# Performance work log

Measured on AMD Instinct MI355X. Metric: run time of the kernel, lower is better.

Reference implementation:

```python
import jax, jax.numpy as jnp
import numpy as np

BS1, BS2, NUM_EC = 32, 128, 64
CONV_DIM, MEM_DIM, MLP_DIM = 64, 256, 256
Q_DIM = 4 * CONV_DIM  # query_dim of criteria


def setup_inputs() -> dict:
    key = jax.random.key(0)
    k = jax.random.split(key, 6)
    in_dim = Q_DIM + MEM_DIM
    s_a = 1.0 / np.sqrt(in_dim)
    return {
        "ehr_vector": jax.random.normal(k[0], (BS2, MEM_DIM), dtype=jnp.float32),
        "criteria": jax.random.normal(k[1], (BS1, NUM_EC, Q_DIM), dtype=jnp.float32),
        "ec_mask": jnp.ones((BS1, NUM_EC), dtype=jnp.float32),
        # alignment: Linear(mem_dim + 4*conv_dim, 1) -> store as [in_dim] vector + scalar bias
        "W_align": jax.random.normal(k[2], (in_dim,), dtype=jnp.float32) * s_a,
        "b_align": jax.random.normal(k[3], (1,), dtype=jnp.float32) * s_a,
        # mlp: Linear(mem_dim + 4*conv_dim, mlp_dim) -> store as [in_dim, mlp_dim]
        "W_mlp": jax.random.normal(k[4], (in_dim, MLP_DIM), dtype=jnp.float32) * s_a,
        "b_mlp": jax.random.normal(k[5], (MLP_DIM,), dtype=jnp.float32) * s_a,
    }


def reference(ehr_vector, criteria, ec_mask, W_align, b_align, W_mlp, b_mlp):
    # Math identical to: att = softmax(Linear(cat[criteria, ehr]), dim=ec);
    # h = Linear_mlp(cat[criteria, ehr] * att). Concat is never materialized:
    # split both linear weights along the input dim instead.
    q = criteria.shape[-1]
    Wa_c, Wa_e = W_align[:q], W_align[q:]
    # additive attention logits: [bs1, bs2, num_ec]
    logit_c = jnp.einsum("beq,q->be", criteria, Wa_c)      # [bs1, num_ec]
    logit_e = jnp.einsum("pm,m->p", ehr_vector, Wa_e)      # [bs2]
    logits = logit_c[:, None, :] + logit_e[None, :, None] + b_align[0]
    att = jax.nn.softmax(logits, axis=2)                   # softmax over num_ec

    Wm_c, Wm_e = W_mlp[:q], W_mlp[q:]
    proj_c = jnp.einsum("beq,qd->bed", criteria, Wm_c)     # [bs1, num_ec, mlp]
    proj_e = jnp.einsum("pm,md->pd", ehr_vector, Wm_e)     # [bs2, mlp]
    # mlp((cat * att)) = att * (cat @ W_mlp) + b_mlp  (att is scalar per (b,p,e))
    h = att[..., None] * (proj_c[:, None, :, :] + proj_e[None, :, None, :]) + b_mlp
    return h  # [bs1, bs2, num_ec, mlp_dim]
```

## Files before the change

### kernel.cpp

```cpp
#include <hip/hip_runtime.h>

#define BS1 32
#define BS2 128
#define NEC 64
#define QD  256
#define MD  256

__global__ __launch_bounds__(256)
void prep_kernel(const float* __restrict__ crit,
                 const float* __restrict__ ehr,
                 const float* __restrict__ w_mlp,
                 const float* __restrict__ w_align,
                 float* __restrict__ proj_c,
                 float* __restrict__ proj_e,
                 float* __restrict__ att) {
    __shared__ float smem[8 * QD];
    __shared__ float logits[NEC];
    int tid = threadIdx.x;
    int blk = blockIdx.x;

    if (blk < 272) {
        const float* A; const float* B; float* out; int m0;
        if (blk < 256) { A = crit; B = w_mlp;           out = proj_c; m0 = blk * 8; }
        else           { A = ehr;  B = w_mlp + QD * MD; out = proj_e; m0 = (blk - 256) * 8; }
        {
            const float* src = A + m0 * QD + tid * 8;
            float4 a0 = *(const float4*)src;
            float4 a1 = *(const float4*)(src + 4);
            *(float4*)&smem[tid * 8]     = a0;
            *(float4*)&smem[tid * 8 + 4] = a1;
        }
        __syncthreads();
        int r = tid >> 5;
        int c = (tid & 31) * 8;
        float acc[8] = {0.f,0.f,0.f,0.f,0.f,0.f,0.f,0.f};
        #pragma unroll 4
        for (int k = 0; k < QD; ++k) {
            float a = smem[r * QD + k];
            const float* bp = B + k * MD + c;
            float4 b0 = *(const float4*)bp;
            float4 b1 = *(const float4*)(bp + 4);
            acc[0] = fmaf(a, b0.x, acc[0]);
            acc[1] = fmaf(a, b0.y, acc[1]);
            acc[2] = fmaf(a, b0.z, acc[2]);
            acc[3] = fmaf(a, b0.w, acc[3]);
            acc[4] = fmaf(a, b1.x, acc[4]);
            acc[5] = fmaf(a, b1.y, acc[5]);
            acc[6] = fmaf(a, b1.z, acc[6]);
            acc[7] = fmaf(a, b1.w, acc[7]);
        }
        float* o = out + (m0 + r) * MD + c;
        *(float4*)o       = make_float4(acc[0], acc[1], acc[2], acc[3]);
        *(float4*)(o + 4) = make_float4(acc[4], acc[5], acc[6], acc[7]);
    } else {
        int b = blk - 272;
        smem[tid] = w_align[tid];
        __syncthreads();
        int e = tid >> 2, q = tid & 3;
        const float* row = crit + (b * NEC + e) * QD + q * 64;
        const float* w   = &smem[q * 64];
        float acc = 0.f;
        #pragma unroll
        for (int k = 0; k < 64; k += 4) {
            float4 u = *(const float4*)(row + k);
            acc = fmaf(u.x, w[k + 0], acc);
            acc = fmaf(u.y, w[k + 1], acc);
            acc = fmaf(u.z, w[k + 2], acc);
            acc = fmaf(u.w, w[k + 3], acc);
        }
        acc += __shfl_xor(acc, 1);
        acc += __shfl_xor(acc, 2);
        if (q == 0) logits[e] = acc;
        __syncthreads();
        if (tid < NEC) {
            float l = logits[tid];
            float m = l;
            #pragma unroll
            for (int off = 32; off; off >>= 1) m = fmaxf(m, __shfl_xor(m, off));
            float ex = __expf(l - m);
            float s = ex;
            #pragma unroll
            for (int off = 32; off; off >>= 1) s += __shfl_xor(s, off);
            att[b * NEC + tid] = ex / s;
        }
    }
}

__global__ __launch_bounds__(256)
void final_kernel(const float* __restrict__ att,
                  const float* __restrict__ proj_c,
                  const float* __restrict__ proj_e,
                  const float* __restrict__ b_mlp,
                  float*       __restrict__ out) {
    int tid = threadIdx.x;
    int bp  = blockIdx.x;
    int b = bp >> 7, p = bp & 127;
    int wid = tid >> 6;
    int d   = (tid & 63) * 4;

    const float4 pe = *(const float4*)(proj_e + p * MD + d);
    const float4 bm = *(const float4*)(b_mlp + d);

    const float* attp = att + b * NEC + wid;
    float a[16];
    #pragma unroll
    for (int pass = 0; pass < 16; ++pass) a[pass] = attp[pass * 4];

    const float* pc = proj_c + (b * NEC + wid) * MD + d;
    float*       o  = out + (size_t)bp * (NEC * MD) + tid * 4;

    #pragma unroll
    for (int pass = 0; pass < 16; ++pass) {
        float4 c0 = *(const float4*)pc;
        float4 r0;
        r0.x = fmaf(a[pass], c0.x + pe.x, bm.x);
        r0.y = fmaf(a[pass], c0.y + pe.y, bm.y);
        r0.z = fmaf(a[pass], c0.z + pe.z, bm.z);
        r0.w = fmaf(a[pass], c0.w + pe.w, bm.w);
        *(float4*)o = r0;
        pc += 4 * MD;
        o  += 1024;
    }
}

extern "C" void kernel_launch(void* const* d_in, const int* in_sizes, int n_in,
                              void* d_out, int out_size, void* d_ws, size_t ws_size,
                              hipStream_t stream) {
    const float* ehr     = (const float*)d_in[0];
    const float* crit    = (const float*)d_in[1];
    const float* w_align = (const float*)d_in[3];
    const float* w_mlp   = (const float*)d_in[5];
    const float* b_mlp   = (const float*)d_in[6];
    float* out = (float*)d_out;

    float* att    = (float*)d_ws;
    float* proj_c = att + BS1 * NEC;
    float* proj_e = proj_c + BS1 * NEC * MD;

    prep_kernel<<<272 + BS1, 256, 0, stream>>>(crit, ehr, w_mlp, w_align,
                                               proj_c, proj_e, att);
    final_kernel<<<BS1 * BS2, 256, 0, stream>>>(att, proj_c, proj_e, b_mlp, out);
}
```

Baseline: 308.8 us.

## Fuse prep and output kernels into one cooperative launch with grid sync

Replaces the two-kernel sequence with a single cooperative kernel of 1024 blocks. The blocks first compute the projections, with the GEMM split into 4-row tiles to spread it over more blocks, plus the attention softmax. After a grid-wide sync, each block writes four (b,p) output slabs. This removes the second launch and the gap between kernels. In exchange it adds a grid barrier and fixes the output phase at 1024 resident blocks, and it falls back to the old two-kernel path if the cooperative launch fails.

```diff
diff --git a/kernel.cpp b/kernel.cpp
--- a/kernel.cpp
+++ b/kernel.cpp
@@ -1,10 +1,117 @@
 #include <hip/hip_runtime.h>
+#include <hip/hip_cooperative_groups.h>
+
+namespace cg = cooperative_groups;
 
 #define BS1 32
 #define BS2 128
 #define NEC 64
 #define QD  256
 #define MD  256
+
+__global__ __launch_bounds__(256, 4)
+void fused_kernel(const float* __restrict__ crit,
+                  const float* __restrict__ ehr,
+                  const float* __restrict__ w_mlp,
+                  const float* __restrict__ w_align,
+                  const float* __restrict__ b_mlp,
+                  float* __restrict__ proj_c,
+                  float* __restrict__ proj_e,
+                  float* __restrict__ att,
+                  float* __restrict__ out) {
+    __shared__ float As[4 * QD];
+    __shared__ float logits[NEC];
+    int tid = threadIdx.x;
+    int blk = blockIdx.x;
+
+    if (blk < 544) {
+        const float* A; const float* B; float* outp; int m0;
+        if (blk < 512) { A = crit; B = w_mlp;           outp = proj_c; m0 = blk * 4; }
+        else           { A = ehr;  B = w_mlp + QD * MD; outp = proj_e; m0 = (blk - 512) * 4; }
+        *(float4*)&As[tid * 4] = *(const float4*)(A + m0 * QD + tid * 4);
+        __syncthreads();
+        int r = tid >> 6;
+        int c = (tid & 63) * 4;
+        float acc[4] = {0.f, 0.f, 0.f, 0.f};
+        #pragma unroll 4
+        for (int k = 0; k < QD; ++k) {
+            float a = As[r * QD + k];
+            float4 b0 = *(const float4*)(B + k * MD + c);
+            acc[0] = fmaf(a, b0.x, acc[0]);
+            acc[1] = fmaf(a, b0.y, acc[1]);
+            acc[2] = fmaf(a, b0.z, acc[2]);
+            acc[3] = fmaf(a, b0.w, acc[3]);
+        }
+        *(float4*)(outp + (m0 + r) * MD + c) =
+            make_float4(acc[0], acc[1], acc[2], acc[3]);
+    } else if (blk < 576) {
+        int b = blk - 544;
+        As[tid] = w_align[tid];
+        __syncthreads();
+        int e = tid >> 2, q = tid & 3;
+        const float* row = crit + (b * NEC + e) * QD + q * 64;
+        const float* w   = &As[q * 64];
+        float acc = 0.f;
+        #pragma unroll
+        for (int k = 0; k < 64; k += 4) {
+            float4 u = *(const float4*)(row + k);
+            acc = fmaf(u.x, w[k + 0], acc);
+            acc = fmaf(u.y, w[k + 1], acc);
+            acc = fmaf(u.z, w[k + 2], acc);
+            acc = fmaf(u.w, w[k + 3], acc);
+        }
+        acc += __shfl_xor(acc, 1);
+        acc += __shfl_xor(acc, 2);
+        if (q == 0) logits[e] = acc;
+        __syncthreads();
+        if (tid < NEC) {
+            float l = logits[tid];
+            float m = l;
+            #pragma unroll
+            for (int off = 32; off; off >>= 1) m = fmaxf(m, __shfl_xor(m, off));
+            float ex = __expf(l - m);
+            float s = ex;
+            #pragma unroll
+            for (int off = 32; off; off >>= 1) s += __shfl_xor(s, off);
+            att[b * NEC + tid] = ex / s;
+        }
+    }
+
+    __threadfence();
+    cg::this_grid().sync();
+
+    int wid = tid >> 6;
+    int d   = (tid & 63) * 4;
+    #pragma unroll
+    for (int i = 0; i < 4; ++i) {
+        int bp = blk + i * 1024;
+        int b = bp >> 7, p = bp & 127;
+
+        const float4 pe = *(const float4*)(proj_e + p * MD + d);
+        const float4 bm = *(const float4*)(b_mlp + d);
+
+        const float* attp = att + b * NEC + wid;
+        float a[16];
+        #pragma unroll
+        for (int pass = 0; pass < 16; ++pass) a[pass] = attp[pass * 4];
+
+        const float* pc = proj_c + (b * NEC + wid) * MD + d;
+        float*       o  = out + (size_t)bp * (NEC * MD) + tid * 4;
+
+        #pragma unroll
+        for (int pass = 0; pass < 16; ++pass) {
+            float4 c0 = *(const float4*)pc;
+            float4 r0;
+            r0.x = fmaf(a[pass], c0.x + pe.x, bm.x);
+            r0.y = fmaf(a[pass], c0.y + pe.y, bm.y);
+            r0.z = fmaf(a[pass], c0.z + pe.z, bm.z);
+            r0.w = fmaf(a[pass], c0.w + pe.w, bm.w);
+            *(float4*)o = r0;
+            pc += 4 * MD;
+            o  += 1024;
+        }
+    }
+}
 
 __global__ __launch_bounds__(256)
 void prep_kernel(const float* __restrict__ crit,
@@ -137,7 +244,16 @@
     float* proj_c = att + BS1 * NEC;
     float* proj_e = proj_c + BS1 * NEC * MD;
 
-    prep_kernel<<<272 + BS1, 256, 0, stream>>>(crit, ehr, w_mlp, w_align,
-                                               proj_c, proj_e, att);
-    final_kernel<<<BS1 * BS2, 256, 0, stream>>>(att, proj_c, proj_e, b_mlp, out);
-}
+    void* args[] = { (void*)&crit, (void*)&ehr, (void*)&w_mlp, (void*)&w_align,
+                     (void*)&b_mlp, (void*)&proj_c, (void*)&proj_e, (void*)&att,
+                     (void*)&out };
+    hipError_t err = hipLaunchCooperativeKernel((void*)fused_kernel,
+                                                dim3(1024), dim3(256),
+                                                args, 0, stream);
+    if (err != hipSuccess) {
+        (void)hipGetLastError();
+        prep_kernel<<<272 + BS1, 256, 0, stream>>>(crit, ehr, w_mlp, w_align,
+                                                   proj_c, proj_e, att);
+        final_kernel<<<BS1 * BS2, 256, 0, stream>>>(att, proj_c, proj_e, b_mlp, out);
+    }
+}
```

New measurement: 511.9 us. +65.8%, slower.

## Remap final kernel blocks to (batch, criterion) and iterate over patients

Applied to the files above, without the earlier changes.

The final kernel's grid changes from one block per (b,p) to one block per (b,e), giving 2048 blocks instead of 4096. Each block computes att*proj_c+b_mlp once and loops over the 128 proj_e rows, four patients per group. This cuts the per-element work to one FMA and reuses the attention scalar and proj_c row from registers. The trade-off is that each wave's output stores now land in rows strided by NEC*MD rather than in one contiguous block, which may hurt write coalescing in this store-bound kernel.

```diff
diff --git a/kernel.cpp b/kernel.cpp
--- a/kernel.cpp
+++ b/kernel.cpp
@@ -93,33 +93,46 @@
                   const float* __restrict__ b_mlp,
                   float*       __restrict__ out) {
     int tid = threadIdx.x;
-    int bp  = blockIdx.x;
-    int b = bp >> 7, p = bp & 127;
-    int wid = tid >> 6;
-    int d   = (tid & 63) * 4;
+    int be  = blockIdx.x;
+    int b = be >> 6, e = be & 63;
+    int w = tid >> 6;
+    int d = (tid & 63) * 4;
 
-    const float4 pe = *(const float4*)(proj_e + p * MD + d);
+    float a = att[b * NEC + e];
+    const float4 pc = *(const float4*)(proj_c + (b * NEC + e) * MD + d);
     const float4 bm = *(const float4*)(b_mlp + d);
+    float4 base;
+    base.x = fmaf(a, pc.x, bm.x);
+    base.y = fmaf(a, pc.y, bm.y);
+    base.z = fmaf(a, pc.z, bm.z);
+    base.w = fmaf(a, pc.w, bm.w);
 
-    const float* attp = att + b * NEC + wid;
-    float a[16];
-    #pragma unroll
-    for (int pass = 0; pass < 16; ++pass) a[pass] = attp[pass * 4];
-
-    const float* pc = proj_c + (b * NEC + wid) * MD + d;
-    float*       o  = out + (size_t)bp * (NEC * MD) + tid * 4;
+    const float* pep = proj_e + w * MD + d;
+    float* o = out + ((size_t)(b * BS2 + w) * NEC + e) * MD + d;
+    const size_t PE_STEP = (size_t)4 * MD;
+    const size_t O_STEP  = (size_t)4 * NEC * MD;
 
     #pragma unroll
-    for (int pass = 0; pass < 16; ++pass) {
-        float4 c0 = *(const float4*)pc;
-        float4 r0;
-        r0.x = fmaf(a[pass], c0.x + pe.x, bm.x);
-        r0.y = fmaf(a[pass], c0.y + pe.y, bm.y);
-        r0.z = fmaf(a[pass], c0.z + pe.z, bm.z);
-        r0.w = fmaf(a[pass], c0.w + pe.w, bm.w);
-        *(float4*)o = r0;
-        pc += 4 * MD;
-        o  += 1024;
+    for (int g = 0; g < 8; ++g) {
+        float4 q0 = *(const float4*)(pep);
+        float4 q1 = *(const float4*)(pep + PE_STEP);
+        float4 q2 = *(const float4*)(pep + 2 * PE_STEP);
+        float4 q3 = *(const float4*)(pep + 3 * PE_STEP);
+        float4 r;
+        r.x = fmaf(a, q0.x, base.x); r.y = fmaf(a, q0.y, base.y);
+        r.z = fmaf(a, q0.z, base.z); r.w = fmaf(a, q0.w, base.w);
+        *(float4*)o = r;
+        r.x = fmaf(a, q1.x, base.x); r.y = fmaf(a, q1.y, base.y);
+        r.z = fmaf(a, q1.z, base.z); r.w = fmaf(a, q1.w, base.w);
+        *(float4*)(o + O_STEP) = r;
+        r.x = fmaf(a, q2.x, base.x); r.y = fmaf(a, q2.y, base.y);
+        r.z = fmaf(a, q2.z, base.z); r.w = fmaf(a, q2.w, base.w);
+        *(float4*)(o + 2 * O_STEP) = r;
+        r.x = fmaf(a, q3.x, base.x); r.y = fmaf(a, q3.y, base.y);
+        r.z = fmaf(a, q3.z, base.z); r.w = fmaf(a, q3.w, base.w);
+        *(float4*)(o + 3 * O_STEP) = r;
+        pep += 4 * PE_STEP;
+        o   += 4 * O_STEP;
     }
 }
 
@@ -139,5 +152,5 @@
 
     prep_kernel<<<272 + BS1, 256, 0, stream>>>(crit, ehr, w_mlp, w_align,
                                                proj_c, proj_e, att);
-    final_kernel<<<BS1 * BS2, 256, 0, stream>>>(att, proj_c, proj_e, b_mlp, out);
+    final_kernel<<<BS1 * NEC, 256, 0, stream>>>(att, proj_c, proj_e, b_mlp, out);
 }
```

Measured after the change: 299.4 us. 1.03x faster.
